# Kernel tuning notes

Hardware: AMD Instinct MI355X
Metric: run time of the kernel (lower is better)

## Reference

```python
import jax, jax.numpy as jnp
import numpy as np

B, N, D, HEAD = 16, 1024, 512, 256  # hidden_size=512, gcn_layer=2 -> head_dim=256


def _xavier(key, shape):
    lim = (6.0 / (shape[0] + shape[-1])) ** 0.5
    return jax.random.uniform(key, shape, jnp.float32, -lim, lim)


def setup_inputs() -> dict:
    key = jax.random.key(0)
    ks = jax.random.split(key, 10)
    fi_lim = (6.0 / (D + 1)) ** 0.5
    return {
        "x": jax.random.normal(ks[0], (B, N, D), jnp.float32),
        "tp_w": _xavier(ks[1], (D, D)), "tp_b": jnp.zeros((D,), jnp.float32),
        "tc_w": _xavier(ks[2], (D, D)), "tc_b": jnp.zeros((D,), jnp.float32),
        "fi_w": jax.random.uniform(ks[3], (D,), jnp.float32, -fi_lim, fi_lim),
        "bil_w": _xavier(ks[4], (D, D)),
        "gcn_w0": _xavier(ks[5], (D, HEAD)), "gcn_b0": jnp.zeros((HEAD,), jnp.float32),
        "gcn_w1": _xavier(ks[6], (D + HEAD, HEAD)), "gcn_b1": jnp.zeros((HEAD,), jnp.float32),
        "out_w": _xavier(ks[7], (D, D)), "out_b": jnp.zeros((D,), jnp.float32),
    }


def reference(x, tp_w, tp_b, tc_w, tc_b, fi_w, bil_w,
              gcn_w0, gcn_b0, gcn_w1, gcn_b1, out_w, out_b):
    Bb, Nn, Dd = x.shape
    # ---- StructInduction: matrix-tree latent structure ----
    tp = jnp.tanh(x @ tp_w + tp_b)                      # [B,N,D]
    tc = jnp.tanh(x @ tc_w + tc_b)                      # [B,N,D]
    # original expands BOTH tp and tc along dim 2 -> f_ij[b,i,j] = s[b,i]
    s = jnp.einsum('bnd,de,bne->bn', tp, bil_w, tc)     # [B,N]
    f_i = jnp.exp(x @ fi_w)                             # [B,N] root scores
    eye = jnp.eye(Nn, dtype=x.dtype)
    A = jnp.exp(s)[:, :, None] * (1.0 - eye)            # [B,N,N], zero diagonal
    col_sum = A.sum(axis=1)                             # [B,N] sum over dim 1
    L = -A + col_sum[:, None, :] * eye                  # Laplacian
    L = L.at[:, 0, :].set(f_i)                          # replace row 0 with root scores
    Linv = jnp.linalg.inv(L)                            # [B,N,N]
    d0 = f_i * Linv[:, :, 0]                            # [B,N]
    diag = jnp.diagonal(Linv, axis1=-2, axis2=-1)       # [B,N]
    tmp1 = A * diag[:, None, :]                         # A[b,i,j]*Linv_diag[b,j]
    tmp2 = A * jnp.swapaxes(Linv, 1, 2)                 # A[b,i,j]*Linv[b,j,i]
    mask1 = jnp.concatenate([jnp.zeros((Nn, 1), x.dtype),
                             jnp.ones((Nn, Nn - 1), x.dtype)], axis=1)  # zero col 0
    mask2 = mask1.T                                     # zero row 0
    dx = mask1 * tmp1 - mask2 * tmp2                    # [B,N,N]
    d = jnp.concatenate([d0[:, None, :], dx], axis=1)   # [B,N+1,N]
    df = jnp.swapaxes(d, 1, 2)                          # [B,N,N+1]
    adj = df[:, :, 1:]                                  # [B,N,N] latent adjacency
    # ---- GraphConvLayer (self_loop=True, dropout = identity / eval) ----
    denom = adj.sum(axis=2, keepdims=True) + 1.0        # [B,N,1]
    outputs = x
    cache = [x]
    outs = []
    for (W, b) in ((gcn_w0, gcn_b0), (gcn_w1, gcn_b1)):
        Ax = adj @ outputs                              # [B,N,in_dim]
        AxW = (Ax @ W + b) + (outputs @ W + b)          # neighbor + self loop
        g = jax.nn.relu(AxW / denom)                    # [B,N,HEAD]
        cache.append(g)
        outputs = jnp.concatenate(cache, axis=2)        # densely connected
        outs.append(g)
    gcn_out = jnp.concatenate(outs, axis=2) + x         # [B,N,D] residual
    return gcn_out @ out_w + out_b
```

## Files before the change

### kernel.cpp

```cpp
#include <hip/hip_runtime.h>
#include <cmath>

#define BN   16384
#define DD   512
#define HEADN 256

typedef unsigned short ushort;
typedef short short8 __attribute__((ext_vector_type(8)));
typedef float floatx4 __attribute__((ext_vector_type(4)));
typedef unsigned short ushort4v __attribute__((ext_vector_type(4)));
typedef unsigned short ushort8v __attribute__((ext_vector_type(8)));

__device__ __forceinline__ ushort f2bf(float v) {
    unsigned int u = __float_as_uint(v);
    unsigned int r = u + 0x7FFFu + ((u >> 16) & 1u);
    return (ushort)(r >> 16);
}
__device__ __forceinline__ float bf2f(ushort u) {
    return __uint_as_float(((unsigned int)u) << 16);
}
__device__ __forceinline__ float tanh_fast(float x) {
    float xc = fminf(fmaxf(x, -15.0f), 15.0f);
    float e = __expf(2.0f * xc);
    return (e - 1.0f) * __builtin_amdgcn_rcpf(e + 1.0f);
}

template <int TM, int TN, int KK, int EPI>
__global__ __launch_bounds__(256) void gemm_lds(
    const ushort* __restrict__ A, int lda,
    const ushort* __restrict__ Bt, int N,
    const float* __restrict__ bias,
    const float* __restrict__ denom,
    const ushort* __restrict__ tcb, int tcld,
    float* __restrict__ s_arr,
    void* __restrict__ Cout, int ldc,
    const ushort* __restrict__ xgb, int xoff, ushort* __restrict__ gout,
    const float* __restrict__ pq_a, const float* __restrict__ pq_f,
    float* __restrict__ Pq, float* __restrict__ Qq)
{
    constexpr int MI = TM / 32;
    constexpr int NI = TN / 32;
    constexpr int ROWS = TM + TN;
    constexpr int CPT = (ROWS * 8) / 256;
    constexpr int MT = 16384 / TM;
    constexpr int MT_PER_BAND = MT / 8;
    constexpr int NK = KK >> 6;
    static_assert(NK >= 2, "need >=2 K-iters for depth-2 pipeline");
    static_assert(CPT == 6, "vmcnt literal below assumes CPT==6");
    __shared__ ushort S[3 * ROWS * 64];

    const int g = blockIdx.x;
    const int band = g & 7, within = g >> 3;
    const int nt = within / MT_PER_BAND;
    const int mt = band * MT_PER_BAND + (within - nt * MT_PER_BAND);
    const int m0 = mt * TM, n0 = nt * TN;
    const int w = threadIdx.x >> 6, L = threadIdx.x & 63;
    const int wr0 = (w >> 1) * (TM / 2), wc0 = (w & 1) * (TN / 2);
    const int lrow = L & 15, quad = L >> 4;

    const ushort* gbase[CPT];
#pragma unroll
    for (int rr = 0; rr < CPT; ++rr) {
        const int chunk = rr * 256 + (w << 6) + L;
        const int row = chunk >> 3, slot = chunk & 7;
        const int ca = slot ^ ((row >> 1) & 7);
        gbase[rr] = (row < TM)
            ? A  + (size_t)(m0 + row) * lda    + (ca << 3)
            : Bt + (size_t)(n0 + row - TM) * KK + (ca << 3);
    }

    floatx4 zero4 = {0.0f, 0.0f, 0.0f, 0.0f};
    floatx4 acc[MI][NI];
#pragma unroll
    for (int i = 0; i < MI; ++i)
#pragma unroll
        for (int j = 0; j < NI; ++j) acc[i][j] = zero4;

    auto stage = [&](int buf, int k0) {
        ushort* Sd = S + buf * (ROWS * 64);
#pragma unroll
        for (int rr = 0; rr < CPT; ++rr) {
            __builtin_amdgcn_global_load_lds(
                (const __attribute__((address_space(1))) unsigned int*)(gbase[rr] + k0),
                (__attribute__((address_space(3))) unsigned int*)(Sd + (rr * 256 + (w << 6)) * 8),
                16, 0, 0);
        }
    };

    stage(0, 0);
    stage(1, 64);
#pragma unroll
    for (int kk = 0; kk < NK; ++kk) {
        if (kk + 1 < NK) {
            asm volatile("s_waitcnt vmcnt(6) lgkmcnt(0)" ::: "memory");
            __builtin_amdgcn_s_barrier();
            __builtin_amdgcn_sched_barrier(0);
        } else {
            __syncthreads();
        }
        if (kk + 2 < NK) stage((kk + 2) % 3, (kk + 2) << 6);

        const ushort* Sc = S + (kk % 3) * (ROWS * 64);
        short8 af[2][MI], bfr[2][NI];
#pragma unroll
        for (int ks = 0; ks < 2; ++ks) {
#pragma unroll
            for (int mi = 0; mi < MI; ++mi) {
                const int row = wr0 + (mi << 4) + lrow;
                const int slot = ((ks << 2) + quad) ^ ((row >> 1) & 7);
                af[ks][mi] = *(const short8*)(Sc + row * 64 + (slot << 3));
            }
#pragma unroll
            for (int ni = 0; ni < NI; ++ni) {
                const int row = TM + wc0 + (ni << 4) + lrow;
                const int slot = ((ks << 2) + quad) ^ ((row >> 1) & 7);
                bfr[ks][ni] = *(const short8*)(Sc + row * 64 + (slot << 3));
            }
        }
#pragma unroll
        for (int ks = 0; ks < 2; ++ks)
#pragma unroll
            for (int mi = 0; mi < MI; ++mi)
#pragma unroll
                for (int ni = 0; ni < NI; ++ni)
                    acc[mi][ni] = __builtin_amdgcn_mfma_f32_16x16x32_bf16(
                        bfr[ks][ni], af[ks][mi], acc[mi][ni], 0, 0, 0);
    }

    if constexpr (EPI == 3) {
#pragma unroll
        for (int mi = 0; mi < MI; ++mi) {
            const int gr = m0 + wr0 + (mi << 4) + lrow;
            float rs = 0.0f;
#pragma unroll
            for (int ni = 0; ni < NI; ++ni) {
                const int gcb = n0 + wc0 + (ni << 4) + (quad << 2);
                ushort4v t4 = *(const ushort4v*)(tcb + (size_t)gr * tcld + gcb);
#pragma unroll
                for (int p = 0; p < 4; ++p) rs += acc[mi][ni][p] * bf2f(t4[p]);
            }
            rs += __shfl_xor(rs, 16);
            rs += __shfl_xor(rs, 32);
            if (quad == 0) atomicAdd(s_arr + gr, rs);
        }
    } else {
        float sP[NI][4], sQ[NI][4];
        if constexpr (EPI == 4) {
#pragma unroll
            for (int ni = 0; ni < NI; ++ni)
#pragma unroll
                for (int p = 0; p < 4; ++p) { sP[ni][p] = 0.f; sQ[ni][p] = 0.f; }
        }
#pragma unroll
        for (int mi = 0; mi < MI; ++mi) {
            const int gr = m0 + wr0 + (mi << 4) + lrow;
            const float rdv = (EPI == 2 || EPI == 4)
                            ? __builtin_amdgcn_rcpf(denom[gr]) : 1.0f;
            float av_r = 0.f, afv_r = 0.f;
            if constexpr (EPI == 4) { av_r = pq_a[gr]; afv_r = av_r * pq_f[gr]; }
#pragma unroll
            for (int ni = 0; ni < NI; ++ni) {
                const int gcb = n0 + wc0 + (ni << 4) + (quad << 2);
                const floatx4 v = acc[mi][ni];
                if constexpr (EPI == 0) {
                    float4 bv = *(const float4*)(bias + gcb);
                    float4 o = {v[0] + bv.x, v[1] + bv.y, v[2] + bv.z, v[3] + bv.w};
                    *(float4*)((float*)Cout + (size_t)gr * ldc + gcb) = o;
                } else if constexpr (EPI == 1) {
                    float4 bv = *(const float4*)(bias + gcb);
                    ushort4v o;
                    o[0] = f2bf(tanh_fast(v[0] + bv.x));
                    o[1] = f2bf(tanh_fast(v[1] + bv.y));
                    o[2] = f2bf(tanh_fast(v[2] + bv.z));
                    o[3] = f2bf(tanh_fast(v[3] + bv.w));
                    *(ushort4v*)((ushort*)Cout + (size_t)gr * ldc + gcb) = o;
                } else {
                    float4 bv = *(const float4*)(bias + gcb);
                    float u0 = (v[0] + 2.0f * bv.x) * rdv; u0 = u0 > 0.0f ? u0 : 0.0f;
                    float u1 = (v[1] + 2.0f * bv.y) * rdv; u1 = u1 > 0.0f ? u1 : 0.0f;
                    float u2 = (v[2] + 2.0f * bv.z) * rdv; u2 = u2 > 0.0f ? u2 : 0.0f;
                    float u3 = (v[3] + 2.0f * bv.w) * rdv; u3 = u3 > 0.0f ? u3 : 0.0f;
                    if (Cout) {
                        ushort4v o;
                        o[0] = f2bf(u0); o[1] = f2bf(u1); o[2] = f2bf(u2); o[3] = f2bf(u3);
                        *(ushort4v*)((ushort*)Cout + (size_t)gr * ldc + gcb) = o;
                    }
                    if (gout) {
                        const size_t gb = (size_t)gr * 512 + xoff + gcb;
                        ushort4v xg = *(const ushort4v*)(xgb + gb);
                        ushort4v o;
                        o[0] = f2bf(u0 + bf2f(xg[0]));
                        o[1] = f2bf(u1 + bf2f(xg[1]));
                        o[2] = f2bf(u2 + bf2f(xg[2]));
                        o[3] = f2bf(u3 + bf2f(xg[3]));
                        *(ushort4v*)(gout + gb) = o;
                    }
                    if constexpr (EPI == 4) {
                        sP[ni][0] += av_r * u0;  sQ[ni][0] += afv_r * u0;
                        sP[ni][1] += av_r * u1;  sQ[ni][1] += afv_r * u1;
                        sP[ni][2] += av_r * u2;  sQ[ni][2] += afv_r * u2;
                        sP[ni][3] += av_r * u3;  sQ[ni][3] += afv_r * u3;
                    }
                }
            }
        }
        if constexpr (EPI == 4) {
            const int bb = m0 >> 10;
#pragma unroll
            for (int ni = 0; ni < NI; ++ni) {
                const int gcb = n0 + wc0 + (ni << 4) + (quad << 2);
#pragma unroll
                for (int p = 0; p < 4; ++p) {
                    float vP = sP[ni][p], vQ = sQ[ni][p];
#pragma unroll
                    for (int o = 1; o < 16; o <<= 1) {
                        vP += __shfl_xor(vP, o);
                        vQ += __shfl_xor(vQ, o);
                    }
                    if (lrow == 0) {
                        atomicAdd(Pq + bb * HEADN + gcb + p, vP);
                        atomicAdd(Qq + bb * HEADN + gcb + p, vQ);
                    }
                }
            }
        }
    }
}

__global__ __launch_bounds__(256) void prep_k(
    const float* __restrict__ x, const float* __restrict__ fiw,
    ushort* __restrict__ xb, float* __restrict__ fdot,
    const float* __restrict__ tp_w, const float* __restrict__ tc_w,
    const float* __restrict__ bilw, const float* __restrict__ ow,
    const float* __restrict__ w0, const float* __restrict__ w1,
    const float* __restrict__ tp_b, const float* __restrict__ tc_b,
    ushort* __restrict__ tptcwT, ushort* __restrict__ bilwT,
    ushort* __restrict__ owT, ushort* __restrict__ w0T,
    ushort* __restrict__ w1T, float* __restrict__ bias2,
    float* __restrict__ zstats, int zcount)
{
    const int blk0 = blockIdx.x;
    if (blk0 < 4096) {
        const int wv = threadIdx.x >> 6, L = threadIdx.x & 63;
        const int r = (blk0 << 2) + wv;
        const float* xr = x + (size_t)r * DD;
        const int c0 = L << 3;
        float4 v0 = *(const float4*)(xr + c0);
        float4 v1 = *(const float4*)(xr + c0 + 4);
        float4 f0 = *(const float4*)(fiw + c0);
        float4 f1 = *(const float4*)(fiw + c0 + 4);
        float d = v0.x * f0.x + v0.y * f0.y + v0.z * f0.z + v0.w * f0.w
                + v1.x * f1.x + v1.y * f1.y + v1.z * f1.z + v1.w * f1.w;
        ushort8v o;
        o[0] = f2bf(v0.x); o[1] = f2bf(v0.y); o[2] = f2bf(v0.z); o[3] = f2bf(v0.w);
        o[4] = f2bf(v1.x); o[5] = f2bf(v1.y); o[6] = f2bf(v1.z); o[7] = f2bf(v1.w);
        *(ushort8v*)(xb + (size_t)r * DD + c0) = o;
#pragma unroll
        for (int off = 32; off > 0; off >>= 1) d += __shfl_xor(d, off);
        if (L == 0) fdot[r] = d;
        return;
    }
    if (blk0 >= 5441) {
        for (int i = (blk0 - 5441) * 256 + threadIdx.x; i < zcount; i += 16 * 256)
            zstats[i] = 0.0f;
        return;
    }
    const int blk = blk0 - 4096;
    if (blk >= 1344) {
        for (int i = threadIdx.x; i < 512; i += 256) {
            bias2[i] = tp_b[i];
            bias2[512 + i] = tc_b[i];
        }
        return;
    }
    const float* W; ushort* Wt; int K, N, local;
    if (blk < 256)       { W = tp_w; Wt = tptcwT;              K = 512; N = 512; local = blk; }
    else if (blk < 512)  { W = tc_w; Wt = tptcwT + 512 * 512;  K = 512; N = 512; local = blk - 256; }
    else if (blk < 768)  { W = bilw; Wt = bilwT;               K = 512; N = 512; local = blk - 512; }
    else if (blk < 1024) { W = ow;   Wt = owT;                 K = 512; N = 512; local = blk - 768; }
    else if (blk < 1152) { W = w0;   Wt = w0T;                 K = 512; N = 256; local = blk - 1024; }
    else                 { W = w1;   Wt = w1T;                 K = 768; N = 256; local = blk - 1152; }

    __shared__ float t[32][33];
    const int nb = N >> 5;
    const int kb = local / nb, nbb = local % nb;
    const int k0 = kb << 5, n0 = nbb << 5;
    const int c = threadIdx.x & 31, r = threadIdx.x >> 5;
#pragma unroll
    for (int i = 0; i < 4; ++i)
        t[r + 8 * i][c] = W[(size_t)(k0 + r + 8 * i) * N + n0 + c];
    __syncthreads();
#pragma unroll
    for (int i = 0; i < 4; ++i)
        Wt[(size_t)(n0 + r + 8 * i) * K + k0 + c] = f2bf(t[c][r + 8 * i]);
}

__global__ __launch_bounds__(256) void batch_pq_f(
    const ushort* __restrict__ V, const float* __restrict__ s_arr,
    const float* __restrict__ fdot,
    float* __restrict__ a, float* __restrict__ f,
    float* __restrict__ P, float* __restrict__ Q,
    float* __restrict__ Sb, float* __restrict__ Hb, int C)
{
    __shared__ float redP[256][4];
    __shared__ float redQ[256][4];
    __shared__ float sSh[4], sHh[4];
    const int b = blockIdx.x >> 4;
    const int chunk = blockIdx.x & 15;
    const int c4cnt = C >> 2;
    const int rg = 256 / c4cnt;
    const int c4 = threadIdx.x & (c4cnt - 1);
    const int sub = threadIdx.x / c4cnt;
    const ushort* Vb = V + (size_t)b * 1024 * C;
    const float* sB = s_arr + (b << 10);
    const float* fB = fdot + (b << 10);
    const int n0 = chunk << 6;
    float4 p = {0, 0, 0, 0}, q = {0, 0, 0, 0};
    float sS = 0.f, sH = 0.f;
    for (int n = n0 + sub; n < n0 + 64; n += rg) {
        const float av = __expf(sB[n]);
        const float fv = __expf(fB[n]);
        const float afv = av * fv;
        if (c4 == 0) {
            a[(b << 10) + n] = av;
            f[(b << 10) + n] = fv;
            sS += av; sH += afv;
        }
        ushort4v u = *(const ushort4v*)(Vb + (size_t)n * C + (c4 << 2));
        float4 v = {bf2f(u[0]), bf2f(u[1]), bf2f(u[2]), bf2f(u[3])};
        p.x += av * v.x; p.y += av * v.y; p.z += av * v.z; p.w += av * v.w;
        q.x += afv * v.x; q.y += afv * v.y; q.z += afv * v.z; q.w += afv * v.w;
    }
    if (c4 == 0) { sSh[sub] = sS; sHh[sub] = sH; }
    redP[threadIdx.x][0] = p.x; redP[threadIdx.x][1] = p.y;
    redP[threadIdx.x][2] = p.z; redP[threadIdx.x][3] = p.w;
    redQ[threadIdx.x][0] = q.x; redQ[threadIdx.x][1] = q.y;
    redQ[threadIdx.x][2] = q.z; redQ[threadIdx.x][3] = q.w;
    __syncthreads();
    if (threadIdx.x == 0) {
        float tS = 0.f, tH = 0.f;
        for (int s = 0; s < rg; ++s) { tS += sSh[s]; tH += sHh[s]; }
        atomicAdd(Sb + b, tS);
        atomicAdd(Hb + b, tH);
    }
    if (sub == 0) {
        for (int s = 1; s < rg; ++s) {
            const int t2 = threadIdx.x + s * c4cnt;
            p.x += redP[t2][0]; p.y += redP[t2][1]; p.z += redP[t2][2]; p.w += redP[t2][3];
            q.x += redQ[t2][0]; q.y += redQ[t2][1]; q.z += redQ[t2][2]; q.w += redQ[t2][3];
        }
        float* Pp = P + b * C + (c4 << 2);
        float* Qp = Q + b * C + (c4 << 2);
        atomicAdd(Pp + 0, p.x); atomicAdd(Pp + 1, p.y);
        atomicAdd(Pp + 2, p.z); atomicAdd(Pp + 3, p.w);
        atomicAdd(Qp + 0, q.x); atomicAdd(Qp + 1, q.y);
        atomicAdd(Qp + 2, q.z); atomicAdd(Qp + 3, q.w);
    }
}

__global__ __launch_bounds__(256) void mix_k(
    const ushort* __restrict__ V, const float* __restrict__ P, const float* __restrict__ Q,
    const float* __restrict__ a, const float* __restrict__ f,
    const float* __restrict__ Sb, const float* __restrict__ Hb,
    ushort* __restrict__ outb, int C, int ldo, int co,
    float* __restrict__ den)
{
    const int idx = blockIdx.x * 256 + threadIdx.x;
    const int c4c = C >> 2;
    const int r = idx / c4c, c4 = idx - r * c4c;
    const int b = r >> 10;
    const float av = a[r], fv = f[r], S = Sb[b], H = Hb[b];
    const float rS = __builtin_amdgcn_rcpf(S);
    const float rH = __builtin_amdgcn_rcpf(H);
    const float beta = av * rS * rH;
    const float alpha = 1.0f - av * rS;
    const float cp = rS - beta * fv;
    if (den && c4 == 0) den[r] = 2.0f - av * fv * rH;
    ushort4v u = *(const ushort4v*)(V + (size_t)r * C + (c4 << 2));
    float4 v = {bf2f(u[0]), bf2f(u[1]), bf2f(u[2]), bf2f(u[3])};
    const float* Pp = P + b * C + (c4 << 2);
    const float* Qp = Q + b * C + (c4 << 2);
    ushort4v o;
    o[0] = f2bf(alpha * v.x + cp * Pp[0] + beta * Qp[0]);
    o[1] = f2bf(alpha * v.y + cp * Pp[1] + beta * Qp[1]);
    o[2] = f2bf(alpha * v.z + cp * Pp[2] + beta * Qp[2]);
    o[3] = f2bf(alpha * v.w + cp * Pp[3] + beta * Qp[3]);
    *(ushort4v*)(outb + (size_t)r * ldo + co + (c4 << 2)) = o;
}

extern "C" void kernel_launch(void* const* d_in, const int* in_sizes, int n_in,
                              void* d_out, int out_size, void* d_ws, size_t ws_size,
                              hipStream_t stream)
{
    (void)in_sizes; (void)n_in; (void)out_size; (void)ws_size;
    const float* x    = (const float*)d_in[0];
    const float* tp_w = (const float*)d_in[1];
    const float* tp_b = (const float*)d_in[2];
    const float* tc_w = (const float*)d_in[3];
    const float* tc_b = (const float*)d_in[4];
    const float* fi_w = (const float*)d_in[5];
    const float* bilw = (const float*)d_in[6];
    const float* w0   = (const float*)d_in[7];
    const float* b0   = (const float*)d_in[8];
    const float* w1   = (const float*)d_in[9];
    const float* b1   = (const float*)d_in[10];
    const float* ow   = (const float*)d_in[11];
    const float* ob   = (const float*)d_in[12];

    char* W = (char*)d_ws;
    ushort* xb    = (ushort*)W;
    ushort* gcnb  = xb;
    ushort* tptcb = (ushort*)(W + ((size_t)16 << 20));
    ushort* Hbuf  = tptcb;
    ushort* g0b   = (ushort*)(W + ((size_t)48 << 20));
    ushort* tptcwT= (ushort*)(W + ((size_t)56 << 20));
    ushort* bilwT = tptcwT + 524288;
    ushort* owT   = bilwT + 262144;
    ushort* w0T   = owT + 262144;
    ushort* w1T   = w0T + 131072;
    float*  bias2 = (float*)(w1T + 196608);
    float* stats  = (float*)(W + ((size_t)60 << 20));
    float* s_arr  = stats;
    float* P0     = s_arr + 16384;
    float* Q0     = P0 + 8192;
    float* P1     = Q0 + 8192;
    float* Q1     = P1 + 4096;
    float* Sb     = Q1 + 4096;
    float* Hb     = Sb + 16;
    const int zcount = 16384 + 2 * 8192 + 2 * 4096 + 32;
    float* fdot   = Hb + 16;
    float* arr_a  = fdot + BN;
    float* arr_f  = arr_a + BN;
    float* arr_den= arr_f + BN;

    prep_k<<<5457, 256, 0, stream>>>(x, fi_w, xb, fdot, tp_w, tc_w, bilw, ow, w0, w1,
                                     tp_b, tc_b, tptcwT, bilwT, owT, w0T, w1T, bias2,
                                     s_arr, zcount);
    gemm_lds<128, 64, 512, 1><<<2048, 256, 0, stream>>>(xb, 512, tptcwT, 1024, bias2,
        nullptr, nullptr, 0, nullptr, tptcb, 1024, nullptr, 0, nullptr,
        nullptr, nullptr, nullptr, nullptr);
    gemm_lds<128, 64, 512, 3><<<1024, 256, 0, stream>>>(tptcb, 1024, bilwT, 512, nullptr,
        nullptr, tptcb + 512, 1024, s_arr, nullptr, 0, nullptr, 0, nullptr,
        nullptr, nullptr, nullptr, nullptr);
    batch_pq_f<<<256, 256, 0, stream>>>(xb, s_arr, fdot, arr_a, arr_f,
                                        P0, Q0, Sb, Hb, 512);
    mix_k<<<8192, 256, 0, stream>>>(xb, P0, Q0, arr_a, arr_f, Sb, Hb,
                                    Hbuf, 512, 768, 0, arr_den);
    gemm_lds<128, 64, 512, 4><<<512, 256, 0, stream>>>(Hbuf, 768, w0T, 256, b0,
        arr_den, nullptr, 0, nullptr, g0b, 256, xb, 0, gcnb,
        arr_a, arr_f, P1, Q1);
    mix_k<<<4096, 256, 0, stream>>>(g0b, P1, Q1, arr_a, arr_f, Sb, Hb,
                                    Hbuf, 256, 768, 512, nullptr);
    gemm_lds<128, 64, 768, 2><<<512, 256, 0, stream>>>(Hbuf, 768, w1T, 256, b1,
        arr_den, nullptr, 0, nullptr, nullptr, 0, xb, 256, gcnb,
        nullptr, nullptr, nullptr, nullptr);
    gemm_lds<128, 64, 512, 0><<<1024, 256, 0, stream>>>(gcnb, 512, owT, 512, ob,
        nullptr, nullptr, 0, nullptr, (float*)d_out, 512, nullptr, 0, nullptr,
        nullptr, nullptr, nullptr, nullptr);
}
```

Before: 236.7 us.

## Reassociate GCN mixing through weights and fuse x-projections into first GEMM

Uses linearity to apply the low-rank mixing (alpha*V + cp*P + beta*Q) after multiplying by W instead of before. This lets x@[w0|w1_top] be computed in the same GEMM as the tp/tc projections, and the per-batch P/Q vectors are projected through W by small kernels. The second layer's GEMM shrinks to K=256 over g0, and the bias, ReLU and residual epilogues move into separate elementwise kernels. It removes the mix_k passes and the K=768 GEMM, but adds extra Z buffers, elementwise kernels and launches, and changes bf16 rounding points.

```diff
diff --git a/kernel.cpp b/kernel.cpp
--- a/kernel.cpp
+++ b/kernel.cpp
@@ -28,15 +28,12 @@
 template <int TM, int TN, int KK, int EPI>
 __global__ __launch_bounds__(256) void gemm_lds(
     const ushort* __restrict__ A, int lda,
-    const ushort* __restrict__ Bt, int N,
+    const ushort* __restrict__ Bt,
     const float* __restrict__ bias,
-    const float* __restrict__ denom,
     const ushort* __restrict__ tcb, int tcld,
     float* __restrict__ s_arr,
     void* __restrict__ Cout, int ldc,
-    const ushort* __restrict__ xgb, int xoff, ushort* __restrict__ gout,
-    const float* __restrict__ pq_a, const float* __restrict__ pq_f,
-    float* __restrict__ Pq, float* __restrict__ Qq)
+    ushort* __restrict__ gout)
 {
     constexpr int MI = TM / 32;
     constexpr int NI = TN / 32;
@@ -144,20 +141,9 @@
             if (quad == 0) atomicAdd(s_arr + gr, rs);
         }
     } else {
-        float sP[NI][4], sQ[NI][4];
-        if constexpr (EPI == 4) {
-#pragma unroll
-            for (int ni = 0; ni < NI; ++ni)
-#pragma unroll
-                for (int p = 0; p < 4; ++p) { sP[ni][p] = 0.f; sQ[ni][p] = 0.f; }
-        }
 #pragma unroll
         for (int mi = 0; mi < MI; ++mi) {
             const int gr = m0 + wr0 + (mi << 4) + lrow;
-            const float rdv = (EPI == 2 || EPI == 4)
-                            ? __builtin_amdgcn_rcpf(denom[gr]) : 1.0f;
-            float av_r = 0.f, afv_r = 0.f;
-            if constexpr (EPI == 4) { av_r = pq_a[gr]; afv_r = av_r * pq_f[gr]; }
 #pragma unroll
             for (int ni = 0; ni < NI; ++ni) {
                 const int gcb = n0 + wc0 + (ni << 4) + (quad << 2);
@@ -166,60 +152,25 @@
                     float4 bv = *(const float4*)(bias + gcb);
                     float4 o = {v[0] + bv.x, v[1] + bv.y, v[2] + bv.z, v[3] + bv.w};
                     *(float4*)((float*)Cout + (size_t)gr * ldc + gcb) = o;
-                } else if constexpr (EPI == 1) {
-                    float4 bv = *(const float4*)(bias + gcb);
+                } else if constexpr (EPI == 6) {
                     ushort4v o;
-                    o[0] = f2bf(tanh_fast(v[0] + bv.x));
-                    o[1] = f2bf(tanh_fast(v[1] + bv.y));
-                    o[2] = f2bf(tanh_fast(v[2] + bv.z));
-                    o[3] = f2bf(tanh_fast(v[3] + bv.w));
+                    o[0] = f2bf(v[0]); o[1] = f2bf(v[1]);
+                    o[2] = f2bf(v[2]); o[3] = f2bf(v[3]);
                     *(ushort4v*)((ushort*)Cout + (size_t)gr * ldc + gcb) = o;
                 } else {
-                    float4 bv = *(const float4*)(bias + gcb);
-                    float u0 = (v[0] + 2.0f * bv.x) * rdv; u0 = u0 > 0.0f ? u0 : 0.0f;
-                    float u1 = (v[1] + 2.0f * bv.y) * rdv; u1 = u1 > 0.0f ? u1 : 0.0f;
-                    float u2 = (v[2] + 2.0f * bv.z) * rdv; u2 = u2 > 0.0f ? u2 : 0.0f;
-                    float u3 = (v[3] + 2.0f * bv.w) * rdv; u3 = u3 > 0.0f ? u3 : 0.0f;
-                    if (Cout) {
+                    if (n0 < 1024) {
+                        float4 bv = *(const float4*)(bias + gcb);
                         ushort4v o;
-                        o[0] = f2bf(u0); o[1] = f2bf(u1); o[2] = f2bf(u2); o[3] = f2bf(u3);
+                        o[0] = f2bf(tanh_fast(v[0] + bv.x));
+                        o[1] = f2bf(tanh_fast(v[1] + bv.y));
+                        o[2] = f2bf(tanh_fast(v[2] + bv.z));
+                        o[3] = f2bf(tanh_fast(v[3] + bv.w));
                         *(ushort4v*)((ushort*)Cout + (size_t)gr * ldc + gcb) = o;
-                    }
-                    if (gout) {
-                        const size_t gb = (size_t)gr * 512 + xoff + gcb;
-                        ushort4v xg = *(const ushort4v*)(xgb + gb);
+                    } else {
                         ushort4v o;
-                        o[0] = f2bf(u0 + bf2f(xg[0]));
-                        o[1] = f2bf(u1 + bf2f(xg[1]));
-                        o[2] = f2bf(u2 + bf2f(xg[2]));
-                        o[3] = f2bf(u3 + bf2f(xg[3]));
-                        *(ushort4v*)(gout + gb) = o;
-                    }
-                    if constexpr (EPI == 4) {
-                        sP[ni][0] += av_r * u0;  sQ[ni][0] += afv_r * u0;
-                        sP[ni][1] += av_r * u1;  sQ[ni][1] += afv_r * u1;
-                        sP[ni][2] += av_r * u2;  sQ[ni][2] += afv_r * u2;
-                        sP[ni][3] += av_r * u3;  sQ[ni][3] += afv_r * u3;
-                    }
-                }
-            }
-        }
-        if constexpr (EPI == 4) {
-            const int bb = m0 >> 10;
-#pragma unroll
-            for (int ni = 0; ni < NI; ++ni) {
-                const int gcb = n0 + wc0 + (ni << 4) + (quad << 2);
-#pragma unroll
-                for (int p = 0; p < 4; ++p) {
-                    float vP = sP[ni][p], vQ = sQ[ni][p];
-#pragma unroll
-                    for (int o = 1; o < 16; o <<= 1) {
-                        vP += __shfl_xor(vP, o);
-                        vQ += __shfl_xor(vQ, o);
-                    }
-                    if (lrow == 0) {
-                        atomicAdd(Pq + bb * HEADN + gcb + p, vP);
-                        atomicAdd(Qq + bb * HEADN + gcb + p, vQ);
+                        o[0] = f2bf(v[0]); o[1] = f2bf(v[1]);
+                        o[2] = f2bf(v[2]); o[3] = f2bf(v[3]);
+                        *(ushort4v*)(gout + (size_t)gr * 512 + (gcb - 1024)) = o;
                     }
                 }
             }
@@ -234,9 +185,9 @@
     const float* __restrict__ bilw, const float* __restrict__ ow,
     const float* __restrict__ w0, const float* __restrict__ w1,
     const float* __restrict__ tp_b, const float* __restrict__ tc_b,
-    ushort* __restrict__ tptcwT, ushort* __restrict__ bilwT,
-    ushort* __restrict__ owT, ushort* __restrict__ w0T,
-    ushort* __restrict__ w1T, float* __restrict__ bias2,
+    ushort* __restrict__ B1, ushort* __restrict__ bilwT,
+    ushort* __restrict__ owT, ushort* __restrict__ w1bT,
+    float* __restrict__ bias2,
     float* __restrict__ zstats, int zcount)
 {
     const int blk0 = blockIdx.x;
@@ -274,12 +225,13 @@
         return;
     }
     const float* W; ushort* Wt; int K, N, local;
-    if (blk < 256)       { W = tp_w; Wt = tptcwT;              K = 512; N = 512; local = blk; }
-    else if (blk < 512)  { W = tc_w; Wt = tptcwT + 512 * 512;  K = 512; N = 512; local = blk - 256; }
-    else if (blk < 768)  { W = bilw; Wt = bilwT;               K = 512; N = 512; local = blk - 512; }
-    else if (blk < 1024) { W = ow;   Wt = owT;                 K = 512; N = 512; local = blk - 768; }
-    else if (blk < 1152) { W = w0;   Wt = w0T;                 K = 512; N = 256; local = blk - 1024; }
-    else                 { W = w1;   Wt = w1T;                 K = 768; N = 256; local = blk - 1152; }
+    if (blk < 256)       { W = tp_w;           Wt = B1;              K = 512; N = 512; local = blk; }
+    else if (blk < 512)  { W = tc_w;           Wt = B1 + 512 * 512;  K = 512; N = 512; local = blk - 256; }
+    else if (blk < 768)  { W = bilw;           Wt = bilwT;           K = 512; N = 512; local = blk - 512; }
+    else if (blk < 1024) { W = ow;             Wt = owT;             K = 512; N = 512; local = blk - 768; }
+    else if (blk < 1152) { W = w0;             Wt = B1 + 1024 * 512; K = 512; N = 256; local = blk - 1024; }
+    else if (blk < 1280) { W = w1;             Wt = B1 + 1280 * 512; K = 512; N = 256; local = blk - 1152; }
+    else                 { W = w1 + 512 * 256; Wt = w1bT;            K = 256; N = 256; local = blk - 1280; }
 
     __shared__ float t[32][33];
     const int nb = N >> 5;
@@ -358,34 +310,145 @@
     }
 }
 
-__global__ __launch_bounds__(256) void mix_k(
-    const ushort* __restrict__ V, const float* __restrict__ P, const float* __restrict__ Q,
+__global__ __launch_bounds__(256) void pqw0_k(
+    const float* __restrict__ P0, const float* __restrict__ Q0,
+    const float* __restrict__ w0, const float* __restrict__ w1,
+    float* __restrict__ PW, float* __restrict__ QW)
+{
+    const int bi = blockIdx.x;
+    const int which = bi >> 5;
+    const int rem = bi & 31;
+    const int b = rem >> 1, half = rem & 1;
+    const int c = threadIdx.x;
+    const float* src = (which ? Q0 : P0) + b * 512;
+    const float* Wm = half ? w1 : w0;
+    float acc = 0.f;
+    for (int k = 0; k < 512; ++k) acc += src[k] * Wm[k * 256 + c];
+    float* dst = (which ? QW : PW) + b * 512 + half * 256 + c;
+    *dst = acc;
+}
+
+__global__ __launch_bounds__(256) void pqw1_k(
+    const float* __restrict__ P1, const float* __restrict__ Q1,
+    const float* __restrict__ w1,
+    float* __restrict__ PW1, float* __restrict__ QW1)
+{
+    const int bi = blockIdx.x;
+    const int which = bi >> 4, b = bi & 15;
+    const int c = threadIdx.x;
+    const float* src = (which ? Q1 : P1) + b * 256;
+    float acc = 0.f;
+    for (int k = 0; k < 256; ++k) acc += src[k] * w1[(size_t)(512 + k) * 256 + c];
+    ((which ? QW1 : PW1) + b * 256)[c] = acc;
+}
+
+__global__ __launch_bounds__(256) void ew0_k(
+    const ushort* __restrict__ Z0, const ushort* __restrict__ xb,
+    ushort* __restrict__ g0b, ushort* __restrict__ gcnb,
     const float* __restrict__ a, const float* __restrict__ f,
     const float* __restrict__ Sb, const float* __restrict__ Hb,
-    ushort* __restrict__ outb, int C, int ldo, int co,
-    float* __restrict__ den)
+    const float* __restrict__ PW, const float* __restrict__ QW,
+    const float* __restrict__ b0,
+    float* __restrict__ P1, float* __restrict__ Q1)
+{
+    __shared__ float redP[4][64][4];
+    __shared__ float redQ[4][64][4];
+    const int blk = blockIdx.x;
+    const int r0 = blk << 6;
+    const int b = r0 >> 10;
+    const int c4 = threadIdx.x & 63;
+    const int sub = threadIdx.x >> 6;
+    const int c = c4 << 2;
+    const float S = Sb[b], H = Hb[b];
+    const float rS = __builtin_amdgcn_rcpf(S);
+    const float rH = __builtin_amdgcn_rcpf(H);
+    float4 bv = *(const float4*)(b0 + c);
+    float4 pw = *(const float4*)(PW + b * 512 + c);
+    float4 qw = *(const float4*)(QW + b * 512 + c);
+    float sP[4] = {0.f, 0.f, 0.f, 0.f}, sQ[4] = {0.f, 0.f, 0.f, 0.f};
+    for (int rr = 0; rr < 16; ++rr) {
+        const int r = r0 + (sub << 4) + rr;
+        const float av = a[r], fv = f[r];
+        const float alpha = 1.0f - av * rS;
+        const float beta = av * rS * rH;
+        const float cpv = rS - beta * fv;
+        const float rdv = __builtin_amdgcn_rcpf(2.0f - av * fv * rH);
+        ushort4v z  = *(const ushort4v*)(Z0 + (size_t)r * 512 + c);
+        ushort4v xg = *(const ushort4v*)(xb + (size_t)r * 512 + c);
+        ushort4v og, oc;
+        float u;
+        u = (alpha * bf2f(z[0]) + cpv * pw.x + beta * qw.x + 2.0f * bv.x) * rdv;
+        u = u > 0.f ? u : 0.f; og[0] = f2bf(u); oc[0] = f2bf(u + bf2f(xg[0]));
+        sP[0] += av * u; sQ[0] += av * fv * u;
+        u = (alpha * bf2f(z[1]) + cpv * pw.y + beta * qw.y + 2.0f * bv.y) * rdv;
+        u = u > 0.f ? u : 0.f; og[1] = f2bf(u); oc[1] = f2bf(u + bf2f(xg[1]));
+        sP[1] += av * u; sQ[1] += av * fv * u;
+        u = (alpha * bf2f(z[2]) + cpv * pw.z + beta * qw.z + 2.0f * bv.z) * rdv;
+        u = u > 0.f ? u : 0.f; og[2] = f2bf(u); oc[2] = f2bf(u + bf2f(xg[2]));
+        sP[2] += av * u; sQ[2] += av * fv * u;
+        u = (alpha * bf2f(z[3]) + cpv * pw.w + beta * qw.w + 2.0f * bv.w) * rdv;
+        u = u > 0.f ? u : 0.f; og[3] = f2bf(u); oc[3] = f2bf(u + bf2f(xg[3]));
+        sP[3] += av * u; sQ[3] += av * fv * u;
+        *(ushort4v*)(g0b  + (size_t)r * 256 + c) = og;
+        *(ushort4v*)(gcnb + (size_t)r * 512 + c) = oc;
+    }
+#pragma unroll
+    for (int p = 0; p < 4; ++p) { redP[sub][c4][p] = sP[p]; redQ[sub][c4][p] = sQ[p]; }
+    __syncthreads();
+    if (sub == 0) {
+#pragma unroll
+        for (int p = 0; p < 4; ++p) {
+            float vP = redP[0][c4][p] + redP[1][c4][p] + redP[2][c4][p] + redP[3][c4][p];
+            float vQ = redQ[0][c4][p] + redQ[1][c4][p] + redQ[2][c4][p] + redQ[3][c4][p];
+            atomicAdd(P1 + b * 256 + c + p, vP);
+            atomicAdd(Q1 + b * 256 + c + p, vQ);
+        }
+    }
+}
+
+__global__ __launch_bounds__(256) void ew1_k(
+    const ushort* __restrict__ Z0, const ushort* __restrict__ Zg,
+    const ushort* __restrict__ xb, ushort* __restrict__ gcnb,
+    const float* __restrict__ a, const float* __restrict__ f,
+    const float* __restrict__ Sb, const float* __restrict__ Hb,
+    const float* __restrict__ PW, const float* __restrict__ QW,
+    const float* __restrict__ PW1, const float* __restrict__ QW1,
+    const float* __restrict__ b1)
 {
     const int idx = blockIdx.x * 256 + threadIdx.x;
-    const int c4c = C >> 2;
-    const int r = idx / c4c, c4 = idx - r * c4c;
+    const int c4 = idx & 63, r = idx >> 6;
     const int b = r >> 10;
+    const int c = c4 << 2;
     const float av = a[r], fv = f[r], S = Sb[b], H = Hb[b];
     const float rS = __builtin_amdgcn_rcpf(S);
     const float rH = __builtin_amdgcn_rcpf(H);
+    const float alpha = 1.0f - av * rS;
     const float beta = av * rS * rH;
-    const float alpha = 1.0f - av * rS;
-    const float cp = rS - beta * fv;
-    if (den && c4 == 0) den[r] = 2.0f - av * fv * rH;
-    ushort4v u = *(const ushort4v*)(V + (size_t)r * C + (c4 << 2));
-    float4 v = {bf2f(u[0]), bf2f(u[1]), bf2f(u[2]), bf2f(u[3])};
-    const float* Pp = P + b * C + (c4 << 2);
-    const float* Qp = Q + b * C + (c4 << 2);
+    const float cpv = rS - beta * fv;
+    const float rdv = __builtin_amdgcn_rcpf(2.0f - av * fv * rH);
+    float4 bv = *(const float4*)(b1 + c);
+    float4 pwa = *(const float4*)(PW + b * 512 + 256 + c);
+    float4 qwa = *(const float4*)(QW + b * 512 + 256 + c);
+    float4 pw1 = *(const float4*)(PW1 + b * 256 + c);
+    float4 qw1 = *(const float4*)(QW1 + b * 256 + c);
+    ushort4v za = *(const ushort4v*)(Z0 + (size_t)r * 512 + 256 + c);
+    ushort4v zg = *(const ushort4v*)(Zg + (size_t)r * 256 + c);
+    ushort4v xg = *(const ushort4v*)(xb + (size_t)r * 512 + 256 + c);
     ushort4v o;
-    o[0] = f2bf(alpha * v.x + cp * Pp[0] + beta * Qp[0]);
-    o[1] = f2bf(alpha * v.y + cp * Pp[1] + beta * Qp[1]);
-    o[2] = f2bf(alpha * v.z + cp * Pp[2] + beta * Qp[2]);
-    o[3] = f2bf(alpha * v.w + cp * Pp[3] + beta * Qp[3]);
-    *(ushort4v*)(outb + (size_t)r * ldo + co + (c4 << 2)) = o;
+    float u;
+    u = (alpha * (bf2f(za[0]) + bf2f(zg[0])) + cpv * (pwa.x + pw1.x)
+       + beta * (qwa.x + qw1.x) + 2.0f * bv.x) * rdv;
+    u = u > 0.f ? u : 0.f; o[0] = f2bf(u + bf2f(xg[0]));
+    u = (alpha * (bf2f(za[1]) + bf2f(zg[1])) + cpv * (pwa.y + pw1.y)
+       + beta * (qwa.y + qw1.y) + 2.0f * bv.y) * rdv;
+    u = u > 0.f ? u : 0.f; o[1] = f2bf(u + bf2f(xg[1]));
+    u = (alpha * (bf2f(za[2]) + bf2f(zg[2])) + cpv * (pwa.z + pw1.z)
+       + beta * (qwa.z + qw1.z) + 2.0f * bv.z) * rdv;
+    u = u > 0.f ? u : 0.f; o[2] = f2bf(u + bf2f(xg[2]));
+    u = (alpha * (bf2f(za[3]) + bf2f(zg[3])) + cpv * (pwa.w + pw1.w)
+       + beta * (qwa.w + qw1.w) + 2.0f * bv.w) * rdv;
+    u = u > 0.f ? u : 0.f; o[3] = f2bf(u + bf2f(xg[3]));
+    *(ushort4v*)(gcnb + (size_t)r * 512 + 256 + c) = o;
 }
 
 extern "C" void kernel_launch(void* const* d_in, const int* in_sizes, int n_in,
@@ -411,15 +474,15 @@
     ushort* xb    = (ushort*)W;
     ushort* gcnb  = xb;
     ushort* tptcb = (ushort*)(W + ((size_t)16 << 20));
-    ushort* Hbuf  = tptcb;
-    ushort* g0b   = (ushort*)(W + ((size_t)48 << 20));
-    ushort* tptcwT= (ushort*)(W + ((size_t)56 << 20));
-    ushort* bilwT = tptcwT + 524288;
+    ushort* Z0b   = (ushort*)(W + ((size_t)48 << 20));
+    ushort* g0b   = (ushort*)(W + ((size_t)64 << 20));
+    ushort* Zgb   = (ushort*)(W + ((size_t)72 << 20));
+    ushort* B1    = (ushort*)(W + ((size_t)80 << 20));
+    ushort* bilwT = B1 + 1536 * 512;
     ushort* owT   = bilwT + 262144;
-    ushort* w0T   = owT + 262144;
-    ushort* w1T   = w0T + 131072;
-    float*  bias2 = (float*)(w1T + 196608);
-    float* stats  = (float*)(W + ((size_t)60 << 20));
+    ushort* w1bT  = owT + 262144;
+    float*  bias2 = (float*)(w1bT + 65536);
+    float* stats  = (float*)(W + ((size_t)84 << 20));
     float* s_arr  = stats;
     float* P0     = s_arr + 16384;
     float* Q0     = P0 + 8192;
@@ -431,30 +494,28 @@
     float* fdot   = Hb + 16;
     float* arr_a  = fdot + BN;
     float* arr_f  = arr_a + BN;
-    float* arr_den= arr_f + BN;
+    float* PW     = arr_f + BN;
+    float* QW     = PW + 8192;
+    float* PW1    = QW + 8192;
+    float* QW1    = PW1 + 4096;
 
     prep_k<<<5457, 256, 0, stream>>>(x, fi_w, xb, fdot, tp_w, tc_w, bilw, ow, w0, w1,
-                                     tp_b, tc_b, tptcwT, bilwT, owT, w0T, w1T, bias2,
+                                     tp_b, tc_b, B1, bilwT, owT, w1bT, bias2,
                                      s_arr, zcount);
-    gemm_lds<128, 64, 512, 1><<<2048, 256, 0, stream>>>(xb, 512, tptcwT, 1024, bias2,
-        nullptr, nullptr, 0, nullptr, tptcb, 1024, nullptr, 0, nullptr,
-        nullptr, nullptr, nullptr, nullptr);
-    gemm_lds<128, 64, 512, 3><<<1024, 256, 0, stream>>>(tptcb, 1024, bilwT, 512, nullptr,
-        nullptr, tptcb + 512, 1024, s_arr, nullptr, 0, nullptr, 0, nullptr,
-        nullptr, nullptr, nullptr, nullptr);
+    gemm_lds<128, 64, 512, 5><<<3072, 256, 0, stream>>>(xb, 512, B1, bias2,
+        nullptr, 0, nullptr, tptcb, 1024, Z0b);
+    gemm_lds<128, 64, 512, 3><<<1024, 256, 0, stream>>>(tptcb, 1024, bilwT, nullptr,
+        tptcb + 512, 1024, s_arr, nullptr, 0, nullptr);
     batch_pq_f<<<256, 256, 0, stream>>>(xb, s_arr, fdot, arr_a, arr_f,
                                         P0, Q0, Sb, Hb, 512);
-    mix_k<<<8192, 256, 0, stream>>>(xb, P0, Q0, arr_a, arr_f, Sb, Hb,
-                                    Hbuf, 512, 768, 0, arr_den);
-    gemm_lds<128, 64, 512, 4><<<512, 256, 0, stream>>>(Hbuf, 768, w0T, 256, b0,
-        arr_den, nullptr, 0, nullptr, g0b, 256, xb, 0, gcnb,
-        arr_a, arr_f, P1, Q1);
-    mix_k<<<4096, 256, 0, stream>>>(g0b, P1, Q1, arr_a, arr_f, Sb, Hb,
-                                    Hbuf, 256, 768, 512, nullptr);
-    gemm_lds<128, 64, 768, 2><<<512, 256, 0, stream>>>(Hbuf, 768, w1T, 256, b1,
-        arr_den, nullptr, 0, nullptr, nullptr, 0, xb, 256, gcnb,
-        nullptr, nullptr, nullptr, nullptr);
-    gemm_lds<128, 64, 512, 0><<<1024, 256, 0, stream>>>(gcnb, 512, owT, 512, ob,
-        nullptr, nullptr, 0, nullptr, (float*)d_out, 512, nullptr, 0, nullptr,
-        nullptr, nullptr, nullptr, nullptr);
-}
+    pqw0_k<<<64, 256, 0, stream>>>(P0, Q0, w0, w1, PW, QW);
+    ew0_k<<<256, 256, 0, stream>>>(Z0b, xb, g0b, gcnb, arr_a, arr_f, Sb, Hb,
+                                   PW, QW, b0, P1, Q1);
+    gemm_lds<128, 64, 256, 6><<<512, 256, 0, stream>>>(g0b, 256, w1bT, nullptr,
+        nullptr, 0, nullptr, Zgb, 256, nullptr);
+    pqw1_k<<<32, 256, 0, stream>>>(P1, Q1, w1, PW1, QW1);
+    ew1_k<<<4096, 256, 0, stream>>>(Z0b, Zgb, xb, gcnb, arr_a, arr_f, Sb, Hb,
+                                    PW, QW, PW1, QW1, b1);
+    gemm_lds<128, 64, 512, 0><<<1024, 256, 0, stream>>>(gcnb, 512, owT, ob,
+        nullptr, 0, nullptr, (float*)d_out, 512, nullptr);
+}
```

Measured after the change: 256.4 us. 1.08x slower.
